# Optimization experiments

Measured on AMD Instinct MI355X. Metric: run time of the kernel, lower is better.

The kernel has to match this reference:

```python
import math
import jax, jax.numpy as jnp
import numpy as np

H, C, PQ, PV = 8, 256, 8, 12   # no_heads, c_hidden, no_qk_points, no_v_points
INF, EPS = 1e5, 1e-8

def quat_to_rot(q):
    w, x, y, z = q[..., 0], q[..., 1], q[..., 2], q[..., 3]
    r = jnp.stack([
        1 - 2*(y*y + z*z), 2*(x*y - w*z),     2*(x*z + w*y),
        2*(x*y + w*z),     1 - 2*(x*x + z*z), 2*(y*z - w*x),
        2*(x*z - w*y),     2*(y*z + w*x),     1 - 2*(x*x + y*y),
    ], axis=-1)
    return r.reshape(q.shape[:-1] + (3, 3))

def setup_inputs() -> dict:
    key = jax.random.key(0)
    ks = jax.random.split(key, 16)
    B, N, CS, CZ = 1, 512, 384, 128
    s = jax.random.normal(ks[0], (B, N, CS), jnp.float32)
    z = jax.random.normal(ks[1], (B, N, N, CZ), jnp.float32) * 0.1
    quat = jax.random.normal(ks[2], (B, N, 4), jnp.float32)
    quat = quat / jnp.linalg.norm(quat, axis=-1, keepdims=True)
    rot = quat_to_rot(quat)                       # [B,N,3,3] valid rotations
    trans = jax.random.normal(ks[3], (B, N, 3), jnp.float32) * 10.0
    mask = jnp.ones((B, N), jnp.float32)
    g = lambda k, sh: jax.random.normal(k, sh, jnp.float32) * 0.02
    params = dict(
        wq=g(ks[4], (CS, H*C)), bq=jnp.zeros((H*C,), jnp.float32),
        wkv=g(ks[5], (CS, 2*H*C)), bkv=jnp.zeros((2*H*C,), jnp.float32),
        wqp=g(ks[6], (CS, H*PQ*3)), bqp=jnp.zeros((H*PQ*3,), jnp.float32),
        wkvp=g(ks[7], (CS, H*(PQ+PV)*3)), bkvp=jnp.zeros((H*(PQ+PV)*3,), jnp.float32),
        wb=g(ks[8], (CZ, H)), bb=jnp.zeros((H,), jnp.float32),
        wz=g(ks[9], (CZ, CZ//4)), bz=jnp.zeros((CZ//4,), jnp.float32),
        head_weights=jnp.full((H,), 0.541324854612918, jnp.float32),  # softplus^-1(1)
        wo=g(ks[10], (H*(C + 4*PV + CZ//4), CS)), bo=jnp.zeros((CS,), jnp.float32),
    )
    return dict(s=s, z=z, rot=rot, trans=trans, mask=mask, **params)

def reference(s, z, rot, trans, mask, wq, bq, wkv, bkv, wqp, bqp, wkvp, bkvp, wb, bb, wz, bz, head_weights, wo, bo):
    B, N, CS = s.shape
    q = (s @ wq + bq).reshape(B, N, H, C)
    kv = (s @ wkv + bkv).reshape(B, N, H, 2 * C)
    k, v = kv[..., :C], kv[..., C:]

    def split_pts(x):  # torch split-into-3 + stack(-1): [B,N,3*M] -> [B,N,M,3]
        return jnp.moveaxis(x.reshape(B, N, 3, -1), -2, -1)

    def apply_rigid(p):  # global frame: R @ p + t
        return jnp.einsum('bnij,bnpj->bnpi', rot, p) + trans[:, :, None, :]

    q_pts = apply_rigid(split_pts(s @ wqp + bqp)).reshape(B, N, H, PQ, 3)
    kv_pts = apply_rigid(split_pts(s @ wkvp + bkvp)).reshape(B, N, H, PQ + PV, 3)
    k_pts, v_pts = kv_pts[..., :PQ, :], kv_pts[..., PQ:, :]

    b_bias = z @ wb + bb                                  # [B,Ni,Nj,H]
    a = jnp.einsum('bihc,bjhc->bhij', q, k) * math.sqrt(1.0 / (3 * C))
    a = a + math.sqrt(1.0 / 3) * jnp.moveaxis(b_bias, -1, 1)

    disp = q_pts[:, :, None] - k_pts[:, None]             # [B,Ni,Nj,H,PQ,3]
    pt_att = jnp.sum(disp * disp, axis=-1)                # [B,Ni,Nj,H,PQ]
    hw = jax.nn.softplus(head_weights) * math.sqrt(1.0 / (3 * (PQ * 9.0 / 2)))
    pt_att = -0.5 * jnp.sum(pt_att * hw[None, None, None, :, None], axis=-1)  # [B,Ni,Nj,H]

    sq_mask = INF * (mask[:, :, None] * mask[:, None, :] - 1.0)
    a = a + jnp.moveaxis(pt_att, -1, 1) + sq_mask[:, None]
    a = jax.nn.softmax(a, axis=-1)                        # [B,H,Ni,Nj]

    o = jnp.einsum('bhij,bjhc->bihc', a, v).reshape(B, N, H * C)

    o_pt = jnp.einsum('bhij,bjhpd->bihpd', a, v_pts)      # [B,N,H,PV,3] global
    o_pt = jnp.einsum('bnji,bnhpj->bnhpi', rot, o_pt - trans[:, :, None, None, :])  # invert_apply
    o_pt_norm = jnp.sqrt(jnp.sum(o_pt * o_pt, axis=-1) + EPS).reshape(B, N, H * PV)
    o_pt_flat = o_pt.reshape(B, N, H * PV, 3)

    pair_z = z @ wz + bz                                  # [B,Ni,Nj,CZ//4]
    o_pair = jnp.einsum('bhij,bijd->bihd', a, pair_z).reshape(B, N, -1)

    feats = jnp.concatenate(
        [o, o_pt_flat[..., 0], o_pt_flat[..., 1], o_pt_flat[..., 2], o_pt_norm, o_pair], axis=-1)
    return feats @ wo + bo
```

## Files before the change

kernel.cpp:

```cpp
#include <hip/hip_runtime.h>


#define OFF_QBH    0
#define OFF_KBH    524288
#define OFF_VB     1048576
#define OFF_QPRAW  2097152
#define OFF_KVPRAW 2195456
#define OFF_BBIAS  2785280
#define OFF_PAIRZT 3833856
#define OFF_ATTNH  8028160
#define OFF_FEATSB 9076736
#define OFF_WCAT   9764864
#define OFF_WTALL  9767936
#define OFF_VPT    11082752
#define OFF_WOT    11803648
#define OFF_QPTH   12319744
#define OFF_QPTL   12385280
#define OFF_KPTH   12450816
#define OFF_KPTL   12516352
#define OFF_QP2    12581888
#define OFF_KP2    12585984
#define OFF_SBF    12590080

typedef __attribute__((ext_vector_type(8))) short short8;
typedef __attribute__((ext_vector_type(4))) float f32x4;

__device__ __forceinline__ unsigned short f2bf(float f) {
  union { float f; unsigned u; } v; v.f = f;
  unsigned u = v.u;
  unsigned r = (u + 0x7fffu + ((u >> 16) & 1u)) >> 16;
  return (unsigned short)r;
}
__device__ __forceinline__ float bf2f(unsigned short h) {
  union { unsigned u; float f; } v; v.u = ((unsigned)h) << 16; return v.f;
}
__device__ __forceinline__ short8 pack8(float4 a, float4 b) {
  short8 r;
  r[0] = (short)f2bf(a.x); r[1] = (short)f2bf(a.y);
  r[2] = (short)f2bf(a.z); r[3] = (short)f2bf(a.w);
  r[4] = (short)f2bf(b.x); r[5] = (short)f2bf(b.y);
  r[6] = (short)f2bf(b.z); r[7] = (short)f2bf(b.w);
  return r;
}
__device__ __forceinline__ void gl_lds16(const float* g, float* l) {
  __builtin_amdgcn_global_load_lds(
      (const __attribute__((address_space(1))) unsigned int*)(g),
      (__attribute__((address_space(3))) unsigned int*)(l), 16, 0, 0);
}

__global__ __launch_bounds__(256) void prep_all(
    const float* __restrict__ wq, const float* __restrict__ wkv,
    const float* __restrict__ wqp, const float* __restrict__ wkvp,
    const float* __restrict__ wo, const float* __restrict__ wb,
    const float* __restrict__ wz, const float* __restrict__ s,
    unsigned short* __restrict__ wTall, unsigned short* __restrict__ woT,
    unsigned short* __restrict__ wT, unsigned short* __restrict__ sbf) {
  __shared__ float tile[64][65];
  const int b = blockIdx.x, t = threadIdx.x;
  if (b < 642) {
    const int ntile = b % 107, kt = b / 107;
    const float* src; int Nsrc, nloc0;
    const int ng0 = ntile * 64;
    if (ntile < 32)      { src = wq;   Nsrc = 2048; nloc0 = ng0; }
    else if (ntile < 96) { src = wkv;  Nsrc = 4096; nloc0 = ng0 - 2048; }
    else if (ntile < 99) { src = wqp;  Nsrc = 192;  nloc0 = ng0 - 6144; }
    else                 { src = wkvp; Nsrc = 480;  nloc0 = ng0 - 6336; }
    const int r = t >> 2, cs = (t & 3) * 16;
#pragma unroll
    for (int i = 0; i < 16; i += 4) {
      int n = nloc0 + cs + i;
      float4 v;
      if (n + 3 < Nsrc) v = *(const float4*)(src + (size_t)(kt * 64 + r) * Nsrc + n);
      else {
        v.x = (n + 0 < Nsrc) ? src[(size_t)(kt * 64 + r) * Nsrc + n + 0] : 0.f;
        v.y = (n + 1 < Nsrc) ? src[(size_t)(kt * 64 + r) * Nsrc + n + 1] : 0.f;
        v.z = (n + 2 < Nsrc) ? src[(size_t)(kt * 64 + r) * Nsrc + n + 2] : 0.f;
        v.w = (n + 3 < Nsrc) ? src[(size_t)(kt * 64 + r) * Nsrc + n + 3] : 0.f;
      }
      tile[r][cs + i + 0] = v.x; tile[r][cs + i + 1] = v.y;
      tile[r][cs + i + 2] = v.z; tile[r][cs + i + 3] = v.w;
    }
    __syncthreads();
    const int nr = t >> 2, ks = (t & 3) * 16;
    unsigned short ov[16];
#pragma unroll
    for (int i = 0; i < 16; i++) ov[i] = f2bf(tile[ks + i][nr]);
    unsigned short* dst = wTall + (size_t)(ng0 + nr) * 384 + kt * 64 + ks;
    *(uint4*)(dst) = *(const uint4*)&ov[0];
    *(uint4*)(dst + 8) = *(const uint4*)&ov[8];
  } else if (b < 894) {
    const int idx = b - 642;
    const int kt = idx % 42, ntile = idx / 42;
    const int r = t >> 2, cs = (t & 3) * 16;
#pragma unroll
    for (int i = 0; i < 16; i += 4) {
      float4 v = *(const float4*)(wo + (size_t)(kt * 64 + r) * 384 + ntile * 64 + cs + i);
      tile[r][cs + i + 0] = v.x; tile[r][cs + i + 1] = v.y;
      tile[r][cs + i + 2] = v.z; tile[r][cs + i + 3] = v.w;
    }
    __syncthreads();
    const int nr = t >> 2, ks = (t & 3) * 16;
    unsigned short ov[16];
#pragma unroll
    for (int i = 0; i < 16; i++) ov[i] = f2bf(tile[ks + i][nr]);
    unsigned short* dst = woT + (size_t)(ntile * 64 + nr) * 2688 + kt * 64 + ks;
    *(uint4*)(dst) = *(const uint4*)&ov[0];
    *(uint4*)(dst + 8) = *(const uint4*)&ov[8];
  } else if (b < 918) {
    const int l = (b - 894) * 256 + t;
    if (l < 6144) {
      int n = l >> 7, k = l & 127;
      float v = (n < 8) ? wb[k * 8 + n] * 0.5773502691896258f
                        : (n < 40 ? wz[k * 32 + (n - 8)] : 0.f);
      wT[l] = f2bf(v);
    }
  } else {
    const int gid = (b - 918) * 256 + t;
    const int off = gid * 8;
    float4 a0 = *(const float4*)(s + off);
    float4 a1 = *(const float4*)(s + off + 4);
    *(short8*)(sbf + off) = pack8(a0, a1);
  }
}

__global__ __launch_bounds__(256) void mega1(
    const float* __restrict__ z, const unsigned short* __restrict__ wT,
    const float* __restrict__ bb, const float* __restrict__ bz,
    unsigned short* __restrict__ bbias_tb, unsigned short* __restrict__ pairzT,
    const unsigned short* __restrict__ sbf, const unsigned short* __restrict__ wTall,
    const float* __restrict__ bq, const float* __restrict__ bkv,
    const float* __restrict__ bqp, const float* __restrict__ bkvp,
    unsigned short* __restrict__ qbh, unsigned short* __restrict__ kbh,
    float* __restrict__ vb, float* __restrict__ qpraw, float* __restrict__ kvpraw) {
  const int lane = threadIdx.x & 63, wv = threadIdx.x >> 6;
  const int quad = lane >> 4, m = lane & 15;
  if (blockIdx.x < 256) {
    __shared__ __align__(16) float zt[2][64][128];
    __shared__ __align__(16) unsigned short lb[4][8][16];
    __shared__ __align__(16) unsigned short lp[4][32][16];
    short8 bfw[3][4];
#pragma unroll
    for (int nt = 0; nt < 3; nt++)
#pragma unroll
      for (int s = 0; s < 4; s++)
        bfw[nt][s] = *(const short8*)(wT + (size_t)(nt * 16 + m) * 128 + s * 32 + quad * 8);
    float bias[3];
#pragma unroll
    for (int nt = 0; nt < 3; nt++) {
      int c = nt * 16 + m;
      bias[nt] = (c < 8) ? 0.5773502691896258f * bb[c] : (c < 40 ? bz[c - 8] : 0.f);
    }
    const int lrow = lane >> 5, lcol = (lane & 31) * 4;
    {
      const int Tg0 = blockIdx.x * 16;
#pragma unroll
      for (int i2 = 0; i2 < 8; i2++) {
        const int k = wv * 8 + i2;
        gl_lds16(z + (size_t)(Tg0 * 64 + 2 * k + lrow) * 128 + lcol, &zt[0][2 * k][0]);
      }
    }
    __syncthreads();
    for (int T = 0; T < 16; T++) {
      const int buf = T & 1;
      const int Tg = blockIdx.x * 16 + T;
      if (T < 15) {
#pragma unroll
        for (int i2 = 0; i2 < 8; i2++) {
          const int k = wv * 8 + i2;
          gl_lds16(z + (size_t)((Tg + 1) * 64 + 2 * k + lrow) * 128 + lcol,
                   &zt[buf ^ 1][2 * k][0]);
        }
      }
      f32x4 acc[3];
#pragma unroll
      for (int nt = 0; nt < 3; nt++) acc[nt] = (f32x4){0.f, 0.f, 0.f, 0.f};
#pragma unroll
      for (int s = 0; s < 4; s++) {
        const float* zr = &zt[buf][wv * 16 + m][s * 32 + quad * 8];
        float4 a0 = *(const float4*)(zr);
        float4 a1 = *(const float4*)(zr + 4);
        short8 af = pack8(a0, a1);
#pragma unroll
        for (int nt = 0; nt < 3; nt++)
          acc[nt] = __builtin_amdgcn_mfma_f32_16x16x32_bf16(af, bfw[nt][s], acc[nt], 0, 0, 0);
      }
#pragma unroll
      for (int nt = 0; nt < 3; nt++) {
        const int c = nt * 16 + m;
#pragma unroll
        for (int r = 0; r < 4; r++) {
          const float v = acc[nt][r] + bias[nt];
          const int jl = quad * 4 + r;
          if (c < 8)       lb[wv][c][jl] = f2bf(v);
          else if (c < 40) lp[wv][c - 8][jl] = f2bf(v);
        }
      }
      const int row0 = Tg * 64 + wv * 16;
      const int i = row0 >> 9, j0 = row0 & 511;
      if (lane < 16) {
        int c = lane >> 1, half = lane & 1;
        uint4 val = *(const uint4*)&lb[wv][c][half * 8];
        *(uint4*)(bbias_tb + (size_t)c * 262144 + row0 + half * 8) = val;
      }
      {
        int d = lane >> 1, half = lane & 1;
        uint4 val = *(const uint4*)&lp[wv][d][half * 8];
        *(uint4*)(pairzT + ((size_t)i * 32 + d) * 512 + j0 + half * 8) = val;
      }
      __syncthreads();
    }
  } else {
    const int b2 = blockIdx.x - 256;
    const int bx = b2 % 107, row0 = (b2 / 107) * 64;
    const int n0 = bx * 64;
    const unsigned short* srow = sbf + (size_t)(row0 + wv * 16 + m) * 384;
    f32x4 acc[4];
#pragma unroll
    for (int nt = 0; nt < 4; nt++) acc[nt] = (f32x4){0.f, 0.f, 0.f, 0.f};
#pragma unroll
    for (int ksx = 0; ksx < 12; ksx++) {
      const int c0 = ksx * 32 + quad * 8;
      short8 af = *(const short8*)(srow + c0);
#pragma unroll
      for (int nt = 0; nt < 4; nt++) {
        short8 bfw2 = *(const short8*)(wTall + (size_t)(n0 + nt * 16 + m) * 384 + c0);
        acc[nt] = __builtin_amdgcn_mfma_f32_16x16x32_bf16(af, bfw2, acc[nt], 0, 0, 0);
      }
    }
    const int rbase = row0 + wv * 16 + quad * 4;
#pragma unroll
    for (int nt = 0; nt < 4; nt++) {
      const int col = n0 + nt * 16 + m;
      if (n0 < 2048) {
        const float bias = bq[col];
#pragma unroll
        for (int r = 0; r < 4; r++)
          qbh[(size_t)(rbase + r) * 2048 + col] = f2bf(acc[nt][r] + bias);
      } else if (n0 < 6144) {
        const int ckv = col - 2048;
        const float bias = bkv[ckv];
        const int hh = ckv >> 9, c = ckv & 511;
        if (c < 256) {
#pragma unroll
          for (int r = 0; r < 4; r++)
            kbh[(size_t)(rbase + r) * 2048 + hh * 256 + c] = f2bf(acc[nt][r] + bias);
        } else {
#pragma unroll
          for (int r = 0; r < 4; r++)
            vb[(size_t)(rbase + r) * 2048 + hh * 256 + (c - 256)] = acc[nt][r] + bias;
        }
      } else if (n0 < 6336) {
        const int cq = col - 6144;
        const float bias = bqp[cq];
#pragma unroll
        for (int r = 0; r < 4; r++)
          qpraw[(size_t)(rbase + r) * 192 + cq] = acc[nt][r] + bias;
      } else {
        const int ck = col - 6336;
        if (ck < 480) {
          const float bias = bkvp[ck];
#pragma unroll
          for (int r = 0; r < 4; r++)
            kvpraw[(size_t)(rbase + r) * 480 + ck] = acc[nt][r] + bias;
        }
      }
    }
  }
}

__global__ __launch_bounds__(256) void mega2(
    const float* __restrict__ vb, const float* __restrict__ qpraw,
    const float* __restrict__ kvpraw, const float* __restrict__ rot,
    const float* __restrict__ trans, unsigned short* __restrict__ vptT,
    unsigned short* __restrict__ qptH, unsigned short* __restrict__ qptL,
    unsigned short* __restrict__ kptH, unsigned short* __restrict__ kptL,
    float* __restrict__ qp2g, float* __restrict__ kp2g) {
  __shared__ float tile[64][65];
  const int b = blockIdx.x, t = threadIdx.x;
  if (b < 320) {
    const int jt = b & 7, h = (b >> 3) & 7, part = b >> 6;
    const int j0 = jt * 64;
    if (part < 4) {
      const int c0 = part * 64;
      const int r = t >> 2, cs = (t & 3) * 16;
#pragma unroll
      for (int ii = 0; ii < 16; ii += 4) {
        float4 v = *(const float4*)(vb + (size_t)(j0 + r) * 2048 + h * 256 + c0 + cs + ii);
        tile[r][cs + ii + 0] = v.x; tile[r][cs + ii + 1] = v.y;
        tile[r][cs + ii + 2] = v.z; tile[r][cs + ii + 3] = v.w;
      }
      __syncthreads();
      const int cl = t >> 2, js = (t & 3) * 16;
      unsigned short ov[16];
#pragma unroll
      for (int x = 0; x < 16; x++) ov[x] = f2bf(tile[js + x][cl]);
      unsigned short* dst = vptT + ((size_t)h * 352 + c0 + cl) * 512 + j0 + js;
      *(uint4*)dst = *(const uint4*)&ov[0];
      *(uint4*)(dst + 8) = *(const uint4*)&ov[8];
    } else {
      float (*lds)[37] = (float(*)[37])&tile[0][0];
      for (int l = t; l < 64 * 36; l += 256) {
        int jl = l / 36, w = l % 36;
        int p = w / 3, d = w % 3;
        const int n = j0 + jl;
        const int pidx = h * 20 + 8 + p;
        const float* kr = kvpraw + (size_t)n * 480;
        float px = kr[pidx], py = kr[160 + pidx], pz = kr[320 + pidx];
        const float* R = rot + n * 9;
        lds[jl][w] = R[d * 3 + 0] * px + R[d * 3 + 1] * py + R[d * 3 + 2] * pz + trans[n * 3 + d];
      }
      __syncthreads();
#pragma unroll
      for (int step = 0; step < 3; step++) {
        int chunk = t + 256 * step;
        int row = chunk >> 3, js = (chunk & 7) * 8;
        unsigned short ov[8];
#pragma unroll
        for (int x = 0; x < 8; x++) {
          int w = (row < 48) ? row : row - 48;
          float f = (w < 36) ? lds[js + x][w] : 0.f;
          unsigned short hi = f2bf(f);
          ov[x] = (row < 48) ? hi : f2bf(f - bf2f(hi));
        }
        *(uint4*)(vptT + ((size_t)h * 352 + 256 + row) * 512 + j0 + js) = *(const uint4*)&ov[0];
      }
    }
  } else {
    const int idx = b - 320;
    const int row = (idx & 1) * 256 + t;
    const int h = idx >> 1;
    const float* R  = rot + row * 9;
    const float* tr = trans + row * 3;
    {
      const float* qr = qpraw + (size_t)row * 192;
      unsigned short hi[32], lo[32]; float s2 = 0.f;
#pragma unroll
      for (int p = 0; p < 8; p++) {
        const int pidx = h * 8 + p;
        float px = qr[pidx], py = qr[64 + pidx], pz = qr[128 + pidx];
        float X = R[0] * px + R[1] * py + R[2] * pz + tr[0];
        float Y = R[3] * px + R[4] * py + R[5] * pz + tr[1];
        float Z = R[6] * px + R[7] * py + R[8] * pz + tr[2];
        hi[p * 3 + 0] = f2bf(X); lo[p * 3 + 0] = f2bf(X - bf2f(hi[p * 3 + 0]));
        hi[p * 3 + 1] = f2bf(Y); lo[p * 3 + 1] = f2bf(Y - bf2f(hi[p * 3 + 1]));
        hi[p * 3 + 2] = f2bf(Z); lo[p * 3 + 2] = f2bf(Z - bf2f(hi[p * 3 + 2]));
        s2 += X * X + Y * Y + Z * Z;
      }
#pragma unroll
      for (int w = 24; w < 32; w++) { hi[w] = 0; lo[w] = 0; }
      unsigned short* dh = qptH + ((size_t)h * 512 + row) * 32;
      unsigned short* dl = qptL + ((size_t)h * 512 + row) * 32;
#pragma unroll
      for (int g = 0; g < 4; g++) {
        *(uint4*)(dh + g * 8) = *(const uint4*)&hi[g * 8];
        *(uint4*)(dl + g * 8) = *(const uint4*)&lo[g * 8];
      }
      qp2g[h * 512 + row] = s2;
    }
    {
      const float* kr = kvpraw + (size_t)row * 480;
      unsigned short hi[32], lo[32]; float s2 = 0.f;
#pragma unroll
      for (int p = 0; p < 8; p++) {
        const int pidx = h * 20 + p;
        float px = kr[pidx], py = kr[160 + pidx], pz = kr[320 + pidx];
        float X = R[0] * px + R[1] * py + R[2] * pz + tr[0];
        float Y = R[3] * px + R[4] * py + R[5] * pz + tr[1];
        float Z = R[6] * px + R[7] * py + R[8] * pz + tr[2];
        hi[p * 3 + 0] = f2bf(X); lo[p * 3 + 0] = f2bf(X - bf2f(hi[p * 3 + 0]));
        hi[p * 3 + 1] = f2bf(Y); lo[p * 3 + 1] = f2bf(Y - bf2f(hi[p * 3 + 1]));
        hi[p * 3 + 2] = f2bf(Z); lo[p * 3 + 2] = f2bf(Z - bf2f(hi[p * 3 + 2]));
        s2 += X * X + Y * Y + Z * Z;
      }
#pragma unroll
      for (int w = 24; w < 32; w++) { hi[w] = 0; lo[w] = 0; }
      unsigned short* dh = kptH + ((size_t)h * 512 + row) * 32;
      unsigned short* dl = kptL + ((size_t)h * 512 + row) * 32;
#pragma unroll
      for (int g = 0; g < 4; g++) {
        *(uint4*)(dh + g * 8) = *(const uint4*)&hi[g * 8];
        *(uint4*)(dl + g * 8) = *(const uint4*)&lo[g * 8];
      }
      kp2g[h * 512 + row] = s2;
    }
  }
}

__global__ __launch_bounds__(512) void logits_fused(
    const unsigned short* __restrict__ qbh, const unsigned short* __restrict__ kbh,
    const unsigned short* __restrict__ qptH, const unsigned short* __restrict__ qptL,
    const unsigned short* __restrict__ kptH, const unsigned short* __restrict__ kptL,
    const float* __restrict__ qp2g, const float* __restrict__ kp2g,
    const unsigned short* __restrict__ bbias_tb, const float* __restrict__ mask,
    const float* __restrict__ hwp, const unsigned short* __restrict__ vptT,
    const float* __restrict__ rot, const float* __restrict__ trans,
    unsigned short* __restrict__ attnh, unsigned short* __restrict__ featsb) {
  const int it = blockIdx.x, h = blockIdx.y;
  const int i0 = it * 16;
  __shared__ __align__(16) unsigned short sth[8][16][72], stl[8][16][72];
  __shared__ float redm[16][8], reds[16][8];
  __shared__ float lds_h[16][48], lds_l[16][48];
  const int t = threadIdx.x;
  const int lane = t & 63, wv = t >> 6;
  const int quad = lane >> 4, m = lane & 15;
  const int jw0 = wv * 64;

  f32x4 acc[4];
#pragma unroll
  for (int nt = 0; nt < 4; nt++) acc[nt] = (f32x4){0.f, 0.f, 0.f, 0.f};
  const unsigned short* qrow = qbh + (size_t)(i0 + m) * 2048 + h * 256;
#pragma unroll
  for (int s = 0; s < 8; s++) {
    short8 af = *(const short8*)(qrow + s * 32 + quad * 8);
#pragma unroll
    for (int nt = 0; nt < 4; nt++) {
      short8 bfr = *(const short8*)(kbh + (size_t)(jw0 + nt * 16 + m) * 2048 + h * 256 + s * 32 + quad * 8);
      acc[nt] = __builtin_amdgcn_mfma_f32_16x16x32_bf16(af, bfr, acc[nt], 0, 0, 0);
    }
  }

  short8 aqh = *(const short8*)(qptH + ((size_t)h * 512 + i0 + m) * 32 + quad * 8);
  short8 aql = *(const short8*)(qptL + ((size_t)h * 512 + i0 + m) * 32 + quad * 8);
  f32x4 accp[4];
#pragma unroll
  for (int nt = 0; nt < 4; nt++) {
    const size_t krow = ((size_t)h * 512 + jw0 + nt * 16 + m) * 32 + quad * 8;
    short8 bkh = *(const short8*)(kptH + krow);
    short8 bkl = *(const short8*)(kptL + krow);
    f32x4 p = (f32x4){0.f, 0.f, 0.f, 0.f};
    p = __builtin_amdgcn_mfma_f32_16x16x32_bf16(aqh, bkh, p, 0, 0, 0);
    p = __builtin_amdgcn_mfma_f32_16x16x32_bf16(aqh, bkl, p, 0, 0, 0);
    p = __builtin_amdgcn_mfma_f32_16x16x32_bf16(aql, bkh, p, 0, 0, 0);
    accp[nt] = p;
  }

  const float c1 = 0.03608439182435161f;
  const float hw = log1pf(expf(hwp[h])) * 0.09622504486493764f;
  float qp2v[4];
#pragma unroll
  for (int r = 0; r < 4; r++) qp2v[r] = qp2g[h * 512 + i0 + quad * 4 + r];
  float lg[4][4];
  float rmax[4] = {-1e30f, -1e30f, -1e30f, -1e30f};
#pragma unroll
  for (int nt = 0; nt < 4; nt++) {
    const int j = jw0 + nt * 16 + m;
    const float kp2v = kp2g[h * 512 + j];
    const float mj = mask[j];
#pragma unroll
    for (int r = 0; r < 4; r++) {
      const int il = quad * 4 + r;
      const float pt = qp2v[r] + kp2v - 2.f * accp[nt][r];
      float v = c1 * acc[nt][r]
              + bf2f(bbias_tb[(size_t)h * 262144 + (size_t)(i0 + il) * 512 + j])
              - 0.5f * hw * pt
              + 100000.f * (mask[i0 + il] * mj - 1.f);
      lg[nt][r] = v;
      rmax[r] = fmaxf(rmax[r], v);
    }
  }
#pragma unroll
  for (int r = 0; r < 4; r++) {
#pragma unroll
    for (int off = 1; off < 16; off <<= 1) rmax[r] = fmaxf(rmax[r], __shfl_xor(rmax[r], off));
  }
  if (m == 0) {
#pragma unroll
    for (int r = 0; r < 4; r++) redm[quad * 4 + r][wv] = rmax[r];
  }
  __syncthreads();
  float rowm[4], rsum[4];
#pragma unroll
  for (int r = 0; r < 4; r++) {
    const int il = quad * 4 + r;
    float m0 = fmaxf(fmaxf(redm[il][0], redm[il][1]), fmaxf(redm[il][2], redm[il][3]));
    float m1 = fmaxf(fmaxf(redm[il][4], redm[il][5]), fmaxf(redm[il][6], redm[il][7]));
    rowm[r] = fmaxf(m0, m1);
    rsum[r] = 0.f;
  }
#pragma unroll
  for (int nt = 0; nt < 4; nt++)
#pragma unroll
    for (int r = 0; r < 4; r++) {
      float e = __expf(lg[nt][r] - rowm[r]);
      lg[nt][r] = e;
      rsum[r] += e;
    }
#pragma unroll
  for (int r = 0; r < 4; r++) {
#pragma unroll
    for (int off = 1; off < 16; off <<= 1) rsum[r] += __shfl_xor(rsum[r], off);
  }
  if (m == 0) {
#pragma unroll
    for (int r = 0; r < 4; r++) reds[quad * 4 + r][wv] = rsum[r];
  }
  __syncthreads();
  float inv[4];
#pragma unroll
  for (int r = 0; r < 4; r++) {
    const int il = quad * 4 + r;
    float s0 = (reds[il][0] + reds[il][1]) + (reds[il][2] + reds[il][3]);
    float s1 = (reds[il][4] + reds[il][5]) + (reds[il][6] + reds[il][7]);
    inv[r] = 1.f / (s0 + s1);
  }
#pragma unroll
  for (int nt = 0; nt < 4; nt++)
#pragma unroll
    for (int r = 0; r < 4; r++) {
      const int il = quad * 4 + r;
      float a = lg[nt][r] * inv[r];
      unsigned short hi = f2bf(a);
      sth[wv][il][nt * 16 + m] = hi;
      stl[wv][il][nt * 16 + m] = f2bf(a - bf2f(hi));
    }
  __syncthreads();
#pragma unroll
  for (int step = 0; step < 2; step++) {
    const int idx = lane + 64 * step;
    const int il = idx >> 3, seg = idx & 7;
    uint4 vh = *(const uint4*)&sth[wv][il][seg * 8];
    *(uint4*)(attnh + ((size_t)h * 512 + i0 + il) * 512 + jw0 + seg * 8) = vh;
  }

  const int nt0 = (wv < 6) ? wv * 3 : 18 + (wv - 6) * 2;
  const int ncnt = (wv < 6) ? 3 : 2;
  f32x4 vacc[3];
#pragma unroll
  for (int k = 0; k < 3; k++) vacc[k] = (f32x4){0.f, 0.f, 0.f, 0.f};
  const unsigned short* vbase = vptT + (size_t)h * 352 * 512;
#pragma unroll
  for (int s = 0; s < 16; s++) {
    const int wsrc = s >> 1, col = (s & 1) * 32 + quad * 8;
    short8 ah = *(const short8*)&sth[wsrc][m][col];
    short8 al = *(const short8*)&stl[wsrc][m][col];
    const int ko = s * 32 + quad * 8;
#pragma unroll
    for (int k = 0; k < 3; k++) {
      if (k < ncnt) {
        const int nt = nt0 + k;
        short8 bfr = *(const short8*)(vbase + (size_t)(nt * 16 + m) * 512 + ko);
        vacc[k] = __builtin_amdgcn_mfma_f32_16x16x32_bf16(ah, bfr, vacc[k], 0, 0, 0);
        if (nt >= 16 && nt < 19)
          vacc[k] = __builtin_amdgcn_mfma_f32_16x16x32_bf16(al, bfr, vacc[k], 0, 0, 0);
      }
    }
  }
#pragma unroll
  for (int k = 0; k < 3; k++) {
    if (k < ncnt) {
      const int nt = nt0 + k;
      if (nt < 16) {
#pragma unroll
        for (int r = 0; r < 4; r++)
          featsb[(size_t)(i0 + quad * 4 + r) * 2688 + h * 256 + nt * 16 + m] = f2bf(vacc[k][r]);
      } else if (nt < 19) {
        const int w = (nt - 16) * 16 + m;
#pragma unroll
        for (int r = 0; r < 4; r++) if (w < 36) lds_h[quad * 4 + r][w] = vacc[k][r];
      } else {
        const int w = (nt - 19) * 16 + m;
#pragma unroll
        for (int r = 0; r < 4; r++) if (w < 36) lds_l[quad * 4 + r][w] = vacc[k][r];
      }
    }
  }
  __syncthreads();
  if (t < 192) {
    const int il = t / 12, p = t % 12, irow = i0 + il;
    const float* R = rot + irow * 9;
    const float* tr = trans + irow * 3;
    float x  = lds_h[il][p * 3 + 0] + lds_l[il][p * 3 + 0] - tr[0];
    float y  = lds_h[il][p * 3 + 1] + lds_l[il][p * 3 + 1] - tr[1];
    float zz = lds_h[il][p * 3 + 2] + lds_l[il][p * 3 + 2] - tr[2];
    float o0 = R[0] * x + R[3] * y + R[6] * zz;
    float o1 = R[1] * x + R[4] * y + R[7] * zz;
    float o2 = R[2] * x + R[5] * y + R[8] * zz;
    float nrm = sqrtf(o0 * o0 + o1 * o1 + o2 * o2 + 1e-8f);
    unsigned short* fr = featsb + (size_t)irow * 2688 + 2048;
    fr[h * 12 + p]       = f2bf(o0);
    fr[96 + h * 12 + p]  = f2bf(o1);
    fr[192 + h * 12 + p] = f2bf(o2);
    fr[288 + h * 12 + p] = f2bf(nrm);
  }
}

__global__ __launch_bounds__(256) void o_pair_mfma(
    const unsigned short* __restrict__ attnh, const unsigned short* __restrict__ pairzT,
    unsigned short* __restrict__ featsb) {
  const int lane = threadIdx.x & 63, wv = threadIdx.x >> 6;
  const int quad = lane >> 4, m = lane & 15;
  const int i = blockIdx.x * 4 + wv;
  f32x4 acc[2];
  acc[0] = (f32x4){0.f, 0.f, 0.f, 0.f};
  acc[1] = (f32x4){0.f, 0.f, 0.f, 0.f};
#pragma unroll
  for (int s = 0; s < 16; s++) {
    const int ko = s * 32 + quad * 8;
    short8 af = *(const short8*)(attnh + (size_t)(m & 7) * 262144 + (size_t)i * 512 + ko);
#pragma unroll
    for (int nt = 0; nt < 2; nt++) {
      short8 bfr = *(const short8*)(pairzT + ((size_t)i * 32 + nt * 16 + m) * 512 + ko);
      acc[nt] = __builtin_amdgcn_mfma_f32_16x16x32_bf16(af, bfr, acc[nt], 0, 0, 0);
    }
  }
  if (quad < 2) {
#pragma unroll
    for (int nt = 0; nt < 2; nt++)
#pragma unroll
      for (int r = 0; r < 4; r++) {
        const int hh = quad * 4 + r, d = nt * 16 + m;
        featsb[(size_t)i * 2688 + 2432 + hh * 32 + d] = f2bf(acc[nt][r]);
      }
  }
}

__global__ __launch_bounds__(256) void out_mfma(
    const unsigned short* __restrict__ featsb, const unsigned short* __restrict__ woT,
    const float* __restrict__ bo, float* __restrict__ out) {
  const int it = blockIdx.x, ng = blockIdx.y;
  const int lane = threadIdx.x & 63, wv = threadIdx.x >> 6;
  const int quad = lane >> 4, m = lane & 15;
  const int i0 = it * 16, n0 = (ng * 4 + wv) * 16;
  const unsigned short* arow = featsb + (size_t)(i0 + m) * 2688;
  const unsigned short* brow = woT + (size_t)(n0 + m) * 2688;
  f32x4 acc = (f32x4){0.f, 0.f, 0.f, 0.f};
#pragma unroll 4
  for (int s = 0; s < 84; s++) {
    const int ko = s * 32 + quad * 8;
    short8 af = *(const short8*)(arow + ko);
    short8 bf = *(const short8*)(brow + ko);
    acc = __builtin_amdgcn_mfma_f32_16x16x32_bf16(af, bf, acc, 0, 0, 0);
  }
  const float bias = bo[n0 + m];
#pragma unroll
  for (int r = 0; r < 4; r++)
    out[(size_t)(i0 + quad * 4 + r) * 384 + n0 + m] = acc[r] + bias;
}

extern "C" void kernel_launch(void* const* d_in, const int* in_sizes, int n_in,
                              void* d_out, int out_size, void* d_ws, size_t ws_size,
                              hipStream_t stream) {
  const float* s     = (const float*)d_in[0];
  const float* z     = (const float*)d_in[1];
  const float* rot   = (const float*)d_in[2];
  const float* trans = (const float*)d_in[3];
  const float* mask  = (const float*)d_in[4];
  const float* wq    = (const float*)d_in[5];
  const float* bq    = (const float*)d_in[6];
  const float* wkv   = (const float*)d_in[7];
  const float* bkv   = (const float*)d_in[8];
  const float* wqp   = (const float*)d_in[9];
  const float* bqp   = (const float*)d_in[10];
  const float* wkvp  = (const float*)d_in[11];
  const float* bkvp  = (const float*)d_in[12];
  const float* wb    = (const float*)d_in[13];
  const float* bb    = (const float*)d_in[14];
  const float* wz    = (const float*)d_in[15];
  const float* bz    = (const float*)d_in[16];
  const float* hwp   = (const float*)d_in[17];
  const float* wo    = (const float*)d_in[18];
  const float* bo    = (const float*)d_in[19];
  float* out = (float*)d_out;

  float* ws = (float*)d_ws;
  unsigned short* qbh   = (unsigned short*)(ws + OFF_QBH);
  unsigned short* kbh   = (unsigned short*)(ws + OFF_KBH);
  float* vb      = ws + OFF_VB;
  float* qpraw   = ws + OFF_QPRAW;
  float* kvpraw  = ws + OFF_KVPRAW;
  unsigned short* bbias_tb = (unsigned short*)(ws + OFF_BBIAS);
  unsigned short* pairzT   = (unsigned short*)(ws + OFF_PAIRZT);
  unsigned short* attnh    = (unsigned short*)(ws + OFF_ATTNH);
  unsigned short* featsb   = (unsigned short*)(ws + OFF_FEATSB);
  unsigned short* wT    = (unsigned short*)(ws + OFF_WCAT);
  unsigned short* wTall = (unsigned short*)(ws + OFF_WTALL);
  unsigned short* vptT  = (unsigned short*)(ws + OFF_VPT);
  unsigned short* woT   = (unsigned short*)(ws + OFF_WOT);
  unsigned short* qptH  = (unsigned short*)(ws + OFF_QPTH);
  unsigned short* qptL  = (unsigned short*)(ws + OFF_QPTL);
  unsigned short* kptH  = (unsigned short*)(ws + OFF_KPTH);
  unsigned short* kptL  = (unsigned short*)(ws + OFF_KPTL);
  float* qp2g = ws + OFF_QP2;
  float* kp2g = ws + OFF_KP2;
  unsigned short* sbf = (unsigned short*)(ws + OFF_SBF);

  prep_all<<<1014, 256, 0, stream>>>(wq, wkv, wqp, wkvp, wo, wb, wz, s,
                                     wTall, woT, wT, sbf);
  mega1<<<1112, 256, 0, stream>>>(z, wT, bb, bz, bbias_tb, pairzT,
                                  sbf, wTall, bq, bkv, bqp, bkvp,
                                  qbh, kbh, vb, qpraw, kvpraw);
  mega2<<<336, 256, 0, stream>>>(vb, qpraw, kvpraw, rot, trans, vptT,
                                 qptH, qptL, kptH, kptL, qp2g, kp2g);
  logits_fused<<<dim3(32, 8), 512, 0, stream>>>(qbh, kbh, qptH, qptL, kptH, kptL,
                                                qp2g, kp2g, bbias_tb, mask, hwp,
                                                vptT, rot, trans, attnh, featsb);
  o_pair_mfma<<<128, 256, 0, stream>>>(attnh, pairzT, featsb);
  out_mfma<<<dim3(32, 6), 256, 0, stream>>>(featsb, woT, bo, out);
}
```

Before: 323.2 us.

## Split-K across waves in o_pair and output GEMMs, remap logits block order

o_pair_mfma now assigns one block per row and splits the 512-long K dimension across four waves, combining their partial sums through shared memory. This quadruples the grid from 128 to 512 blocks. out_mfma doubles the block to 512 threads and splits K in two halves that are reduced in LDS, giving more waves per tile. logits_fused uses a 1D grid with the head index varying fastest, which changes the order blocks are scheduled. The aim is better CU occupancy and latency hiding on small grids, paid for with extra LDS traffic and __syncthreads.

```diff
diff --git a/kernel.cpp b/kernel.cpp
--- a/kernel.cpp
+++ b/kernel.cpp
@@ -395,7 +395,8 @@
     const float* __restrict__ hwp, const unsigned short* __restrict__ vptT,
     const float* __restrict__ rot, const float* __restrict__ trans,
     unsigned short* __restrict__ attnh, unsigned short* __restrict__ featsb) {
-  const int it = blockIdx.x, h = blockIdx.y;
+  const int bx = blockIdx.x;
+  const int h = bx & 7, it = bx >> 3;
   const int i0 = it * 16;
   __shared__ __align__(16) unsigned short sth[8][16][72], stl[8][16][72];
   __shared__ float redm[16][8], reds[16][8];
@@ -589,12 +590,14 @@
     unsigned short* __restrict__ featsb) {
   const int lane = threadIdx.x & 63, wv = threadIdx.x >> 6;
   const int quad = lane >> 4, m = lane & 15;
-  const int i = blockIdx.x * 4 + wv;
+  const int i = blockIdx.x;
+  __shared__ float red[4][2][64][4];
   f32x4 acc[2];
   acc[0] = (f32x4){0.f, 0.f, 0.f, 0.f};
   acc[1] = (f32x4){0.f, 0.f, 0.f, 0.f};
 #pragma unroll
-  for (int s = 0; s < 16; s++) {
+  for (int s4 = 0; s4 < 4; s4++) {
+    const int s = wv * 4 + s4;
     const int ko = s * 32 + quad * 8;
     short8 af = *(const short8*)(attnh + (size_t)(m & 7) * 262144 + (size_t)i * 512 + ko);
 #pragma unroll
@@ -603,38 +606,55 @@
       acc[nt] = __builtin_amdgcn_mfma_f32_16x16x32_bf16(af, bfr, acc[nt], 0, 0, 0);
     }
   }
-  if (quad < 2) {
+#pragma unroll
+  for (int nt = 0; nt < 2; nt++)
+#pragma unroll
+    for (int r = 0; r < 4; r++) red[wv][nt][lane][r] = acc[nt][r];
+  __syncthreads();
+  if (wv == 0 && quad < 2) {
 #pragma unroll
     for (int nt = 0; nt < 2; nt++)
 #pragma unroll
       for (int r = 0; r < 4; r++) {
+        float sum = (red[0][nt][lane][r] + red[1][nt][lane][r])
+                  + (red[2][nt][lane][r] + red[3][nt][lane][r]);
         const int hh = quad * 4 + r, d = nt * 16 + m;
-        featsb[(size_t)i * 2688 + 2432 + hh * 32 + d] = f2bf(acc[nt][r]);
-      }
-  }
-}
-
-__global__ __launch_bounds__(256) void out_mfma(
+        featsb[(size_t)i * 2688 + 2432 + hh * 32 + d] = f2bf(sum);
+      }
+  }
+}
+
+__global__ __launch_bounds__(512) void out_mfma(
     const unsigned short* __restrict__ featsb, const unsigned short* __restrict__ woT,
     const float* __restrict__ bo, float* __restrict__ out) {
   const int it = blockIdx.x, ng = blockIdx.y;
-  const int lane = threadIdx.x & 63, wv = threadIdx.x >> 6;
+  const int t = threadIdx.x;
+  const int lane = t & 63, w8 = t >> 6;
+  const int wn = w8 & 3, wk = w8 >> 2;
   const int quad = lane >> 4, m = lane & 15;
-  const int i0 = it * 16, n0 = (ng * 4 + wv) * 16;
-  const unsigned short* arow = featsb + (size_t)(i0 + m) * 2688;
-  const unsigned short* brow = woT + (size_t)(n0 + m) * 2688;
+  const int i0 = it * 16, n0 = (ng * 4 + wn) * 16;
+  const unsigned short* arow = featsb + (size_t)(i0 + m) * 2688 + wk * 1344;
+  const unsigned short* brow = woT + (size_t)(n0 + m) * 2688 + wk * 1344;
   f32x4 acc = (f32x4){0.f, 0.f, 0.f, 0.f};
-#pragma unroll 4
-  for (int s = 0; s < 84; s++) {
+#pragma unroll 6
+  for (int s = 0; s < 42; s++) {
     const int ko = s * 32 + quad * 8;
     short8 af = *(const short8*)(arow + ko);
     short8 bf = *(const short8*)(brow + ko);
     acc = __builtin_amdgcn_mfma_f32_16x16x32_bf16(af, bf, acc, 0, 0, 0);
   }
-  const float bias = bo[n0 + m];
-#pragma unroll
-  for (int r = 0; r < 4; r++)
-    out[(size_t)(i0 + quad * 4 + r) * 384 + n0 + m] = acc[r] + bias;
+  __shared__ float red[4][64][4];
+  if (wk == 1) {
+#pragma unroll
+    for (int r = 0; r < 4; r++) red[wn][lane][r] = acc[r];
+  }
+  __syncthreads();
+  if (wk == 0) {
+    const float bias = bo[n0 + m];
+#pragma unroll
+    for (int r = 0; r < 4; r++)
+      out[(size_t)(i0 + quad * 4 + r) * 384 + n0 + m] = acc[r] + red[wn][lane][r] + bias;
+  }
 }
 
 extern "C" void kernel_launch(void* const* d_in, const int* in_sizes, int n_in,
@@ -691,9 +711,9 @@
                                   qbh, kbh, vb, qpraw, kvpraw);
   mega2<<<336, 256, 0, stream>>>(vb, qpraw, kvpraw, rot, trans, vptT,
                                  qptH, qptL, kptH, kptL, qp2g, kp2g);
-  logits_fused<<<dim3(32, 8), 512, 0, stream>>>(qbh, kbh, qptH, qptL, kptH, kptL,
-                                                qp2g, kp2g, bbias_tb, mask, hwp,
-                                                vptT, rot, trans, attnh, featsb);
-  o_pair_mfma<<<128, 256, 0, stream>>>(attnh, pairzT, featsb);
-  out_mfma<<<dim3(32, 6), 256, 0, stream>>>(featsb, woT, bo, out);
-}
+  logits_fused<<<256, 512, 0, stream>>>(qbh, kbh, qptH, qptL, kptH, kptL,
+                                        qp2g, kp2g, bbias_tb, mask, hwp,
+                                        vptT, rot, trans, attnh, featsb);
+  o_pair_mfma<<<512, 256, 0, stream>>>(attnh, pairzT, featsb);
+  out_mfma<<<dim3(32, 6), 512, 0, stream>>>(featsb, woT, bo, out);
+}
```

Result: no change. 320.1 us (-1.0%).
